# Performance work log

Hardware: AMD Instinct MI355X
Metric: run time of the kernel (lower is better)

Reference implementation:

```python
import jax, jax.numpy as jnp
import numpy as np

N_COARSE = 40962   # ico level-6 vertex count
N_NEW = 122880     # level-7 minus level-6 vertices
C_IN = 256
C_OUT = 256


def setup_inputs() -> dict:
    key = jax.random.key(0)
    k1, k2, k3, k4 = jax.random.split(key, 4)
    x = jax.random.normal(k1, (N_COARSE, C_IN), dtype=jnp.float32)
    unpooling_index = jax.random.randint(k2, (N_NEW, 2), 0, N_COARSE, dtype=jnp.int64)
    # nn.Linear params: weight [out, in], bias [out]
    W = jax.random.normal(k3, (C_OUT, C_IN), dtype=jnp.float32) * (1.0 / np.sqrt(C_IN))
    b = jax.random.normal(k4, (C_OUT,), dtype=jnp.float32) * 0.01
    return {"x": x, "unpooling_index": unpooling_index, "W": W, "b": b}


def reference(x, unpooling_index, W, b):
    # Gather the two parent vertices of each new vertex and average them.
    x_up = (x[unpooling_index[:, 0]] + x[unpooling_index[:, 1]]) * 0.5  # [N_NEW, C_IN]
    x_full = jnp.concatenate([x, x_up], axis=0)                          # [N_COARSE+N_NEW, C_IN]
    # nn.Linear: y = x @ W^T + b
    return x_full @ W.T + b
```

## Files before the change

kernel.cpp:

```cpp
#include <hip/hip_runtime.h>
#include <hip/hip_bf16.h>

#define N_COARSE 40962
#define N_NEW    122880
#define M_TOTAL  163842
#define CIN      256
#define COUT     256

#define BM    64
#define MT    ((M_TOTAL + BM - 1) / BM)

#define XB_BYTES ((size_t)N_COARSE * CIN * 2)
#define WB_OFF   ((XB_BYTES + 255) & ~(size_t)255)
#define WB_BYTES ((size_t)COUT * CIN * 2)
#define WS_NEED  (WB_OFF + WB_BYTES)

#define XCH   (N_COARSE * CIN / 8)
#define WCH   (COUT * CIN / 8)
#define CVT_T (XCH + WCH)

typedef __bf16 bf16x8 __attribute__((ext_vector_type(8)));
typedef float  f32x4  __attribute__((ext_vector_type(4)));

static __device__ __forceinline__ unsigned short f2bf(float f) {
    unsigned int u = __builtin_bit_cast(unsigned int, f);
    u += 0x7FFFu + ((u >> 16) & 1u);
    return (unsigned short)(u >> 16);
}

__global__ __launch_bounds__(256) void conv_kernel(
    const float* __restrict__ x, const float* __restrict__ W,
    unsigned short* __restrict__ xb, unsigned short* __restrict__ wb2)
{
    const int k = blockIdx.x * 256 + threadIdx.x;
    if (k >= CVT_T) return;
    const float* src;
    unsigned short* dst;
    if (k < XCH) {
        src = x + (size_t)k * 8;
        dst = xb + (size_t)k * 8;
    } else {
        const int o  = k - XCH;
        const int l  = o & 63;
        const int ks = (o >> 6) & 7;
        const int f  = (o >> 9) & 3;
        const int q  = (o >> 11) & 3;
        const int row = q * 64 + f * 16 + (l & 15);
        const int ke  = ks * 32 + ((l >> 4) << 3);
        src = W + (size_t)row * CIN + ke;
        dst = wb2 + (size_t)o * 8;
    }
    float4 v0 = *(const float4*)(src);
    float4 v1 = *(const float4*)(src + 4);
    union { unsigned short h[8]; int4 v; } p;
    p.h[0] = f2bf(v0.x); p.h[1] = f2bf(v0.y); p.h[2] = f2bf(v0.z); p.h[3] = f2bf(v0.w);
    p.h[4] = f2bf(v1.x); p.h[5] = f2bf(v1.y); p.h[6] = f2bf(v1.z); p.h[7] = f2bf(v1.w);
    *(int4*)dst = p.v;
}

__global__ __launch_bounds__(512, 6) void fused_gemm_kernel(
    const unsigned short* __restrict__ xb,
    const int*   __restrict__ idx,
    const unsigned short* __restrict__ wb2,
    const float* __restrict__ bias,
    float*       __restrict__ out)
{
    __shared__ __align__(16) unsigned short As[BM * CIN];

    const int brow = blockIdx.x * BM;
    const int t    = threadIdx.x;
    const int lane = t & 63;
    const int wid  = t >> 6;
    const int wrr  = wid >> 2;
    const int wcc  = wid & 3;

    {
        const int r  = t >> 3;
        const int q  = t & 7;
        const int gr = brow + r;
        char* arow = (char*)As + r * 512;
        const int swz = (r & 7) << 4;
        const int cb0 = q * 64;
        if (gr < N_COARSE || gr >= M_TOTAL) {
            const int sr = (gr < N_COARSE) ? gr : 0;
            const char* s = (const char*)xb + (size_t)sr * 512 + cb0;
#pragma unroll
            for (int c = 0; c < 4; ++c)
                *(int4*)(arow + ((cb0 + c * 16) ^ swz)) = *(const int4*)(s + c * 16);
        } else {
            const int j  = gr - N_COARSE;
            const int p0 = idx[2 * j];
            const int p1 = idx[2 * j + 1];
            const char* s0 = (const char*)xb + (size_t)p0 * 512 + cb0;
            const char* s1 = (const char*)xb + (size_t)p1 * 512 + cb0;
#pragma unroll
            for (int c = 0; c < 4; ++c) {
                int4 a = *(const int4*)(s0 + c * 16);
                int4 b = *(const int4*)(s1 + c * 16);
                const unsigned int* au = (const unsigned int*)&a;
                const unsigned int* bu = (const unsigned int*)&b;
                union { unsigned short h[8]; int4 v; } p;
#pragma unroll
                for (int e = 0; e < 4; ++e) {
                    const float alo = __builtin_bit_cast(float, au[e] << 16);
                    const float ahi = __builtin_bit_cast(float, au[e] & 0xFFFF0000u);
                    const float blo = __builtin_bit_cast(float, bu[e] << 16);
                    const float bhi = __builtin_bit_cast(float, bu[e] & 0xFFFF0000u);
                    p.h[2 * e]     = f2bf((alo + blo) * 0.5f);
                    p.h[2 * e + 1] = f2bf((ahi + bhi) * 0.5f);
                }
                *(int4*)(arow + ((cb0 + c * 16) ^ swz)) = p.v;
            }
        }
    }

    f32x4 acc[4][2];
#pragma unroll
    for (int j = 0; j < 4; ++j)
#pragma unroll
        for (int i = 0; i < 2; ++i)
            acc[j][i] = (f32x4){0.f, 0.f, 0.f, 0.f};

    __syncthreads();

    const char* wbase = (const char*)wb2 + wcc * 32768 + lane * 16;

#pragma unroll
    for (int ks = 0; ks < 8; ++ks) {
        bf16x8 af[2], wf[4];
        const int acb = ks * 64 + ((lane >> 4) << 4);
#pragma unroll
        for (int i = 0; i < 2; ++i) {
            const int ar = wrr * 32 + i * 16 + (lane & 15);
            af[i] = __builtin_bit_cast(bf16x8,
                *(const int4*)((const char*)As + ar * 512 + (acb ^ ((ar & 7) << 4))));
        }
#pragma unroll
        for (int jj = 0; jj < 4; ++jj)
            wf[jj] = *(const bf16x8*)(wbase + jj * 8192 + ks * 1024);

#pragma unroll
        for (int jj = 0; jj < 4; ++jj) {
            acc[jj][0] = __builtin_amdgcn_mfma_f32_16x16x32_bf16(
                wf[jj], af[0], acc[jj][0], 0, 0, 0);
            acc[jj][1] = __builtin_amdgcn_mfma_f32_16x16x32_bf16(
                wf[jj], af[1], acc[jj][1], 0, 0, 0);
        }
    }

    const int nb = wcc * 64 + ((lane >> 4) << 2);
#pragma unroll
    for (int j = 0; j < 4; ++j) {
        const f32x4 bv = __builtin_bit_cast(f32x4, *(const float4*)(bias + nb + j * 16));
#pragma unroll
        for (int i = 0; i < 2; ++i)
            acc[j][i] = acc[j][i] + bv;
    }

    float* Af = (float*)As;
    for (int h = 0; h < 2; ++h) {
        __syncthreads();
        if (wrr == h) {
#pragma unroll
            for (int j = 0; j < 4; ++j)
#pragma unroll
                for (int i = 0; i < 2; ++i) {
                    const int r  = i * 16 + (lane & 15);
                    const int cb = wcc * 256 + j * 64 + ((lane >> 4) << 4);
                    *(f32x4*)((char*)Af + r * 1024 + (cb ^ ((r & 7) << 4))) = acc[j][i];
                }
        }
        __syncthreads();
#pragma unroll
        for (int ri = 0; ri < 4; ++ri) {
            const int r = wid * 4 + ri;
            const f32x4 v = *(const f32x4*)((const char*)Af + r * 1024 +
                                            ((lane * 16) ^ ((r & 7) << 4)));
            const int gr = brow + h * 32 + r;
            if (gr < M_TOTAL)
                *(f32x4*)((char*)out + (size_t)gr * 1024 + lane * 16) = v;
        }
    }
}

union Pk8 { unsigned short h[8]; int4 v; };

__global__ __launch_bounds__(256, 2) void unpool_linear_fused(
    const float* __restrict__ x, const int* __restrict__ idx,
    const float* __restrict__ W, const float* __restrict__ bias,
    float* __restrict__ out)
{
    __shared__ __align__(16) unsigned short As[128 * 64];
    __shared__ __align__(16) unsigned short Bs[128 * 64];
    const int m0 = blockIdx.x * 128;
    const int n0 = blockIdx.y * 128;
    const int t = threadIdx.x, lane = t & 63, wid = t >> 6;
    const int wr = wid >> 1, wc = wid & 1;
    f32x4 acc[4][4];
#pragma unroll
    for (int i = 0; i < 4; ++i)
#pragma unroll
        for (int j = 0; j < 4; ++j) acc[i][j] = (f32x4){0.f,0.f,0.f,0.f};
    for (int k0 = 0; k0 < CIN; k0 += 64) {
#pragma unroll
        for (int i = 0; i < 4; ++i) {
            const int chunk = t + i * 256, r = chunk >> 3, c8 = chunk & 7;
            const int kcol = k0 + c8 * 8;
            const int sidx = (r * 64 + c8 * 8) ^ ((r & 7) << 3);
            float v[8];
            const int gr = m0 + r;
            if (gr < N_COARSE) {
                const float* src = x + (size_t)gr * CIN + kcol;
                float4 a0 = *(const float4*)(src), a1 = *(const float4*)(src + 4);
                v[0]=a0.x; v[1]=a0.y; v[2]=a0.z; v[3]=a0.w;
                v[4]=a1.x; v[5]=a1.y; v[6]=a1.z; v[7]=a1.w;
            } else if (gr < M_TOTAL) {
                const int j = gr - N_COARSE;
                const int p0 = idx[2*j], p1 = idx[2*j+1];
                const float* s0 = x + (size_t)p0 * CIN + kcol;
                const float* s1 = x + (size_t)p1 * CIN + kcol;
                float4 a0=*(const float4*)(s0), a1=*(const float4*)(s0+4);
                float4 b0=*(const float4*)(s1), b1=*(const float4*)(s1+4);
                v[0]=(a0.x+b0.x)*.5f; v[1]=(a0.y+b0.y)*.5f; v[2]=(a0.z+b0.z)*.5f; v[3]=(a0.w+b0.w)*.5f;
                v[4]=(a1.x+b1.x)*.5f; v[5]=(a1.y+b1.y)*.5f; v[6]=(a1.z+b1.z)*.5f; v[7]=(a1.w+b1.w)*.5f;
            } else {
#pragma unroll
                for (int q = 0; q < 8; ++q) v[q] = 0.f;
            }
            Pk8 pa;
#pragma unroll
            for (int q = 0; q < 8; ++q) pa.h[q] = f2bf(v[q]);
            *(int4*)&As[sidx] = pa.v;
            const float* ws = W + (size_t)(n0 + r) * CIN + kcol;
            float4 w0 = *(const float4*)(ws), w1 = *(const float4*)(ws + 4);
            Pk8 pb;
            pb.h[0]=f2bf(w0.x); pb.h[1]=f2bf(w0.y); pb.h[2]=f2bf(w0.z); pb.h[3]=f2bf(w0.w);
            pb.h[4]=f2bf(w1.x); pb.h[5]=f2bf(w1.y); pb.h[6]=f2bf(w1.z); pb.h[7]=f2bf(w1.w);
            *(int4*)&Bs[sidx] = pb.v;
        }
        __syncthreads();
#pragma unroll
        for (int kk = 0; kk < 64; kk += 32) {
            const int kcol = kk + 8 * (lane >> 4);
            bf16x8 af[4], bfv[4];
#pragma unroll
            for (int i = 0; i < 4; ++i) {
                const int r = wr * 64 + i * 16 + (lane & 15);
                af[i] = __builtin_bit_cast(bf16x8, *(const int4*)&As[(r*64+kcol) ^ ((r&7)<<3)]);
            }
#pragma unroll
            for (int j = 0; j < 4; ++j) {
                const int r = wc * 64 + j * 16 + (lane & 15);
                bfv[j] = __builtin_bit_cast(bf16x8, *(const int4*)&Bs[(r*64+kcol) ^ ((r&7)<<3)]);
            }
#pragma unroll
            for (int i = 0; i < 4; ++i)
#pragma unroll
                for (int j = 0; j < 4; ++j)
                    acc[i][j] = __builtin_amdgcn_mfma_f32_16x16x32_bf16(af[i], bfv[j], acc[i][j], 0, 0, 0);
        }
        __syncthreads();
    }
    const int colbase = n0 + wc * 64 + (lane & 15);
    const int rowbase = m0 + wr * 64 + ((lane >> 4) << 2);
#pragma unroll
    for (int j = 0; j < 4; ++j) {
        const int col = colbase + j * 16;
        const float bv = bias[col];
#pragma unroll
        for (int i = 0; i < 4; ++i) {
            const int row = rowbase + i * 16;
#pragma unroll
            for (int r2 = 0; r2 < 4; ++r2) {
                const int rr = row + r2;
                if (rr < M_TOTAL) out[(size_t)rr * COUT + col] = acc[i][j][r2] + bv;
            }
        }
    }
}

extern "C" void kernel_launch(void* const* d_in, const int* in_sizes, int n_in,
                              void* d_out, int out_size, void* d_ws, size_t ws_size,
                              hipStream_t stream) {
    const float* x    = (const float*)d_in[0];
    const int*   idx  = (const int*)d_in[1];
    const float* W    = (const float*)d_in[2];
    const float* bias = (const float*)d_in[3];
    float* out = (float*)d_out;

    if (ws_size >= WS_NEED) {
        unsigned short* xb  = (unsigned short*)d_ws;
        unsigned short* wb2 = (unsigned short*)((char*)d_ws + WB_OFF);
        conv_kernel<<<(CVT_T + 255) / 256, 256, 0, stream>>>(x, W, xb, wb2);
        fused_gemm_kernel<<<MT, 512, 0, stream>>>(xb, idx, wb2, bias, out);
    } else {
        dim3 grid((M_TOTAL + 127) / 128, COUT / 128);
        unpool_linear_fused<<<grid, 256, 0, stream>>>(x, idx, W, bias, out);
    }
}
```

Baseline: 75.25 us.

## Bucket-sort new vertices by parent index to improve gather locality

Adds a counting-sort pipeline (zero histogram, histogram, scan, scatter) that groups new vertices by the high bits of their first parent index, then has the fused GEMM tile over the sorted order and scatter output rows back to their original positions. The goal is better cache locality for the random bf16 row gathers. It adds four small kernel launches, atomics, and an extra metadata read per row, and the output writes become row-scattered rather than contiguous.

After: 300.9 us. 300% more time.

```diff
diff --git a/kernel.cpp b/kernel.cpp
--- a/kernel.cpp
+++ b/kernel.cpp
@@ -7,13 +7,22 @@
 #define CIN      256
 #define COUT     256
 
-#define BM    64
-#define MT    ((M_TOTAL + BM - 1) / BM)
-
-#define XB_BYTES ((size_t)N_COARSE * CIN * 2)
-#define WB_OFF   ((XB_BYTES + 255) & ~(size_t)255)
-#define WB_BYTES ((size_t)COUT * CIN * 2)
-#define WS_NEED  (WB_OFF + WB_BYTES)
+#define BM      64
+#define CT      ((N_COARSE + BM - 1) / BM)
+#define NT      (N_NEW / BM)
+#define MT      (CT + NT)
+
+#define NB      64
+#define BSH     10
+
+#define XB_BYTES  ((size_t)N_COARSE * CIN * 2)
+#define WB_OFF    XB_BYTES
+#define WB_BYTES  ((size_t)COUT * CIN * 2)
+#define SORT_OFF  (WB_OFF + WB_BYTES)
+#define SORT_BYTES ((size_t)N_NEW * 16)
+#define HIST_OFF  (SORT_OFF + SORT_BYTES)
+#define CURS_OFF  (HIST_OFF + 256)
+#define WS_NEED   (CURS_OFF + 256)
 
 #define XCH   (N_COARSE * CIN / 8)
 #define WCH   (COUT * CIN / 8)
@@ -26,6 +35,51 @@
     unsigned int u = __builtin_bit_cast(unsigned int, f);
     u += 0x7FFFu + ((u >> 16) & 1u);
     return (unsigned short)(u >> 16);
+}
+
+__global__ __launch_bounds__(64) void zero_hist_kernel(int* __restrict__ hist) {
+    hist[threadIdx.x] = 0;
+}
+
+__global__ __launch_bounds__(256) void hist_kernel(
+    const int* __restrict__ idx, int* __restrict__ hist)
+{
+    __shared__ int h[NB];
+    const int t = threadIdx.x;
+    if (t < NB) h[t] = 0;
+    __syncthreads();
+    const int j = blockIdx.x * 256 + t;
+    if (j < N_NEW) atomicAdd(&h[idx[2 * j] >> BSH], 1);
+    __syncthreads();
+    if (t < NB && h[t]) atomicAdd(&hist[t], h[t]);
+}
+
+__global__ __launch_bounds__(64) void scan_kernel(
+    const int* __restrict__ hist, int* __restrict__ cursor)
+{
+    __shared__ int s[NB];
+    const int t = threadIdx.x;
+    s[t] = hist[t];
+    __syncthreads();
+    if (t == 0) {
+        int acc = 0;
+#pragma unroll
+        for (int i = 0; i < NB; ++i) { const int v = s[i]; s[i] = acc; acc += v; }
+    }
+    __syncthreads();
+    cursor[t] = s[t];
+}
+
+__global__ __launch_bounds__(256) void scatter_kernel(
+    const int* __restrict__ idx, int* __restrict__ cursor,
+    int4* __restrict__ sorted4)
+{
+    const int j = blockIdx.x * 256 + threadIdx.x;
+    if (j >= N_NEW) return;
+    const int p0 = idx[2 * j];
+    const int p1 = idx[2 * j + 1];
+    const int pos = atomicAdd(&cursor[p0 >> BSH], 1);
+    sorted4[pos] = (int4){p0, p1, j, 0};
 }
 
 __global__ __launch_bounds__(256) void conv_kernel(
@@ -60,14 +114,15 @@
 
 __global__ __launch_bounds__(512, 6) void fused_gemm_kernel(
     const unsigned short* __restrict__ xb,
-    const int*   __restrict__ idx,
+    const int4*  __restrict__ sorted4,
     const unsigned short* __restrict__ wb2,
     const float* __restrict__ bias,
     float*       __restrict__ out)
 {
     __shared__ __align__(16) unsigned short As[BM * CIN];
 
-    const int brow = blockIdx.x * BM;
+    const int tile = blockIdx.x;
+    const bool is_new = (tile >= CT);
     const int t    = threadIdx.x;
     const int lane = t & 63;
     const int wid  = t >> 6;
@@ -77,22 +132,21 @@
     {
         const int r  = t >> 3;
         const int q  = t & 7;
-        const int gr = brow + r;
         char* arow = (char*)As + r * 512;
         const int swz = (r & 7) << 4;
         const int cb0 = q * 64;
-        if (gr < N_COARSE || gr >= M_TOTAL) {
+        if (!is_new) {
+            const int gr = tile * BM + r;
             const int sr = (gr < N_COARSE) ? gr : 0;
             const char* s = (const char*)xb + (size_t)sr * 512 + cb0;
 #pragma unroll
             for (int c = 0; c < 4; ++c)
                 *(int4*)(arow + ((cb0 + c * 16) ^ swz)) = *(const int4*)(s + c * 16);
         } else {
-            const int j  = gr - N_COARSE;
-            const int p0 = idx[2 * j];
-            const int p1 = idx[2 * j + 1];
-            const char* s0 = (const char*)xb + (size_t)p0 * 512 + cb0;
-            const char* s1 = (const char*)xb + (size_t)p1 * 512 + cb0;
+            const int sidx = (tile - CT) * BM + r;
+            const int4 meta = sorted4[sidx];
+            const char* s0 = (const char*)xb + (size_t)meta.x * 512 + cb0;
+            const char* s1 = (const char*)xb + (size_t)meta.y * 512 + cb0;
 #pragma unroll
             for (int c = 0; c < 4; ++c) {
                 int4 a = *(const int4*)(s0 + c * 16);
@@ -176,8 +230,17 @@
             const int r = wid * 4 + ri;
             const f32x4 v = *(const f32x4*)((const char*)Af + r * 1024 +
                                             ((lane * 16) ^ ((r & 7) << 4)));
-            const int gr = brow + h * 32 + r;
-            if (gr < M_TOTAL)
+            int gr;
+            bool ok;
+            if (!is_new) {
+                gr = tile * BM + h * 32 + r;
+                ok = (gr < N_COARSE);
+            } else {
+                const int sidx = (tile - CT) * BM + h * 32 + r;
+                gr = N_COARSE + sorted4[sidx].z;
+                ok = true;
+            }
+            if (ok)
                 *(f32x4*)((char*)out + (size_t)gr * 1024 + lane * 16) = v;
         }
     }
@@ -291,8 +354,16 @@
     if (ws_size >= WS_NEED) {
         unsigned short* xb  = (unsigned short*)d_ws;
         unsigned short* wb2 = (unsigned short*)((char*)d_ws + WB_OFF);
+        int4* sorted4 = (int4*)((char*)d_ws + SORT_OFF);
+        int*  hist    = (int*)((char*)d_ws + HIST_OFF);
+        int*  cursor  = (int*)((char*)d_ws + CURS_OFF);
+
+        zero_hist_kernel<<<1, 64, 0, stream>>>(hist);
+        hist_kernel<<<(N_NEW + 255) / 256, 256, 0, stream>>>(idx, hist);
+        scan_kernel<<<1, 64, 0, stream>>>(hist, cursor);
+        scatter_kernel<<<(N_NEW + 255) / 256, 256, 0, stream>>>(idx, cursor, (int4*)sorted4);
         conv_kernel<<<(CVT_T + 255) / 256, 256, 0, stream>>>(x, W, xb, wb2);
-        fused_gemm_kernel<<<MT, 512, 0, stream>>>(xb, idx, wb2, bias, out);
+        fused_gemm_kernel<<<MT, 512, 0, stream>>>(xb, sorted4, wb2, bias, out);
     } else {
         dim3 grid((M_TOTAL + 127) / 128, COUT / 128);
         unpool_linear_fused<<<grid, 256, 0, stream>>>(x, idx, W, bias, out);
```
